# Kernel optimization log

Hardware: AMD Instinct MI355X
Metric: run time of the kernel (lower is better)

Reference implementation:

```python
import jax, jax.numpy as jnp
import numpy as np

B, S, T, V, E, H, D, A = 16, 128, 128, 32000, 512, 512, 512, 512
ENC = 2 * H  # bidirectional encoder output dim
NEG = -1e9


def _w(key, shape, scale=0.05):
    return scale * jax.random.normal(key, shape, dtype=jnp.float32)


def setup_inputs() -> dict:
    key = jax.random.key(0)
    ks = jax.random.split(key, 26)
    src = jax.random.randint(ks[0], (B, S), 1, V)
    tgt = jax.random.randint(ks[1], (B, T), 1, V)
    src_lens = jnp.full((B,), S, dtype=jnp.int32)  # full-length sequences (pack == identity)
    return dict(
        src=src, src_lens=src_lens, tgt=tgt,
        enc_embed=_w(ks[2], (V, E)).at[0].set(0.0),   # padding_idx=0
        Wih_f=_w(ks[3], (4 * H, E)), Whh_f=_w(ks[4], (4 * H, H)),
        bih_f=_w(ks[5], (4 * H,)), bhh_f=_w(ks[6], (4 * H,)),
        Wih_b=_w(ks[7], (4 * H, E)), Whh_b=_w(ks[8], (4 * H, H)),
        bih_b=_w(ks[9], (4 * H,)), bhh_b=_w(ks[10], (4 * H,)),
        Wbh=_w(ks[11], (D, 2 * H)), bbh=_w(ks[12], (D,)),
        Wbc=_w(ks[13], (D, 2 * H)), bbc=_w(ks[14], (D,)),
        Wh_att=_w(ks[15], (A, ENC)), Ws_att=_w(ks[16], (A, D)), v_att=_w(ks[17], (A,)),
        dec_embed=_w(ks[18], (V, E)).at[0].set(0.0),  # padding_idx=0
        Wih_d=_w(ks[19], (4 * D, E + ENC)), Whh_d=_w(ks[20], (4 * D, D)),
        bih_d=_w(ks[21], (4 * D,)), bhh_d=_w(ks[22], (4 * D,)),
        Wfc=_w(ks[23], (V, D + ENC)), bfc=_w(ks[24], (V,)),
    )


def _lstm_cell(x, h, c, Wih, Whh, bih, bhh):
    # PyTorch gate order: i, f, g, o
    g = x @ Wih.T + h @ Whh.T + (bih + bhh)
    i, f, gg, o = jnp.split(g, 4, axis=-1)
    c = jax.nn.sigmoid(f) * c + jax.nn.sigmoid(i) * jnp.tanh(gg)
    h = jax.nn.sigmoid(o) * jnp.tanh(c)
    return h, c


def _run_lstm(xs, Wih, Whh, bih, bhh, hdim):
    # xs: [S, B, E] -> (hs [S, B, hdim], h_last, c_last)
    b = xs.shape[1]
    h0 = jnp.zeros((b, hdim), xs.dtype)

    def step(carry, x):
        h, c = carry
        h, c = _lstm_cell(x, h, c, Wih, Whh, bih, bhh)
        return (h, c), h

    (hT, cT), hs = jax.lax.scan(step, (h0, h0), xs)
    return hs, hT, cT


def reference(src, src_lens, tgt, enc_embed, Wih_f, Whh_f, bih_f, bhh_f,
              Wih_b, Whh_b, bih_b, bhh_b, Wbh, bbh, Wbc, bbc,
              Wh_att, Ws_att, v_att, dec_embed, Wih_d, Whh_d, bih_d, bhh_d,
              Wfc, bfc):
    # ---- BiLSTM encoder (src_lens == S, so packing is the identity) ----
    emb = enc_embed[src]                      # [B, S, E]
    xs = jnp.swapaxes(emb, 0, 1)              # [S, B, E]
    hs_f, hf, _ = _run_lstm(xs, Wih_f, Whh_f, bih_f, bhh_f, H)
    hs_b, hb, _ = _run_lstm(xs[::-1], Wih_b, Whh_b, bih_b, bhh_b, H)
    hs_b = hs_b[::-1]
    enc_out = jnp.swapaxes(jnp.concatenate([hs_f, hs_b], axis=-1), 0, 1)  # [B, S, 2H]

    # ---- bridge (num_layers = 1) ----
    h_cat = jnp.concatenate([hf, hb], axis=-1)  # [B, 2H]
    h0 = jnp.tanh(h_cat @ Wbh.T + bbh)          # [B, D]
    c_cat = jnp.concatenate([hf, hb], axis=-1)
    c0 = jnp.tanh(c_cat @ Wbc.T + bbc)

    mask = jnp.arange(S)[None, :] < src_lens[:, None]  # [B, S]
    enc_proj = jnp.einsum('bse,ae->bsa', enc_out, Wh_att)  # W_h(enc_out), hoisted

    # ---- decoder loop, teacher_forcing = 1.0 ----
    def dec_step(carry, inp_t):
        h, c = carry
        # Bahdanau attention on top-layer hidden state
        score = jnp.einsum('bsa,a->bs', jnp.tanh(enc_proj + (h @ Ws_att.T)[:, None, :]), v_att)
        score = jnp.where(mask, score, NEG)
        attn = jax.nn.softmax(score, axis=-1)
        ctx = jnp.einsum('bs,bse->be', attn, enc_out)       # [B, 2H]
        x = jnp.concatenate([dec_embed[inp_t], ctx], axis=-1)  # [B, E+2H]
        h, c = _lstm_cell(x, h, c, Wih_d, Whh_d, bih_d, bhh_d)
        logits = jnp.concatenate([h, ctx], axis=-1) @ Wfc.T + bfc  # [B, V]
        return (h, c), logits

    inps = tgt[:, :-1].T  # [T-1, B]
    _, logits = jax.lax.scan(dec_step, (h0, c0), inps)
    return jnp.swapaxes(logits, 0, 1)  # [B, T-1, V]
```

## Files before the change

### kernel.cpp

```cpp
#include <hip/hip_runtime.h>

typedef __bf16 bf16x8 __attribute__((ext_vector_type(8)));
typedef float f32x4 __attribute__((ext_vector_type(4)));
typedef unsigned short us;
typedef unsigned long long ull;

#define DEV static __device__ __forceinline__

DEV float bf2f(us u){ union { unsigned u; float f; } x; x.u = ((unsigned)u) << 16; return x.f; }
DEV us f2bf(float f){
  union { float f; unsigned u; } x; x.f = f;
  unsigned r = x.u + 0x7fffu + ((x.u >> 16) & 1u);
  return (us)(r >> 16);
}
DEV unsigned pack2(us lo, us hi){ return (unsigned)lo | ((unsigned)hi << 16); }
DEV float sigm(float x){ return 1.0f / (1.0f + expf(-x)); }
DEV float tanh_fast(float x){ float e = __expf(2.0f * x); return 1.0f - 2.0f / (e + 1.0f); }
DEV void unpk2(unsigned u, float& a, float& b){ a = bf2f((us)u); b = bf2f((us)(u >> 16)); }

DEV unsigned ld4v(const unsigned* p){ return __hip_atomic_load(p, __ATOMIC_RELAXED, __HIP_MEMORY_SCOPE_AGENT); }
DEV ull ld8v(const void* p){ return __hip_atomic_load((const ull*)p, __ATOMIC_RELAXED, __HIP_MEMORY_SCOPE_AGENT); }
DEV void st4v(unsigned* p, unsigned v){ __hip_atomic_store(p, v, __ATOMIC_RELAXED, __HIP_MEMORY_SCOPE_AGENT); }

DEV void gridbar3(unsigned* arr, unsigned ep){
  __syncthreads();
  if (threadIdx.x == 0)
    __hip_atomic_store(arr + (size_t)blockIdx.x * 16, ep, __ATOMIC_RELEASE, __HIP_MEMORY_SCOPE_AGENT);
  if (threadIdx.x < 128){
    while (__hip_atomic_load(arr + (size_t)threadIdx.x * 16, __ATOMIC_RELAXED, __HIP_MEMORY_SCOPE_AGENT) < ep)
      __builtin_amdgcn_s_sleep(4);
  }
  __syncthreads();
}

DEV void groupbar(unsigned* gbase, int slot, unsigned ep){
  __syncthreads();
  if (threadIdx.x == 0)
    __hip_atomic_store(gbase + slot * 16, ep, __ATOMIC_RELEASE, __HIP_MEMORY_SCOPE_AGENT);
  if (threadIdx.x < 8){
    while (__hip_atomic_load(gbase + threadIdx.x * 16, __ATOMIC_RELAXED, __HIP_MEMORY_SCOPE_AGENT) < ep)
      __builtin_amdgcn_s_sleep(2);
  }
  __syncthreads();
}

__global__ void k_f2bf(const float4* __restrict__ in, uint2* __restrict__ out, long n4){
  long stride = (long)gridDim.x * blockDim.x;
  for (long i = (long)blockIdx.x * blockDim.x + threadIdx.x; i < n4; i += stride){
    float4 v = in[i];
    uint2 o; o.x = pack2(f2bf(v.x), f2bf(v.y)); o.y = pack2(f2bf(v.z), f2bf(v.w));
    out[i] = o;
  }
}

__global__ void k_bias3(const float* a0, const float* b0, float* o0,
                        const float* a1, const float* b1, float* o1,
                        const float* a2, const float* b2, float* o2){
  int i = blockIdx.x * 256 + threadIdx.x;
  o0[i] = a0[i] + b0[i];
  o1[i] = a1[i] + b1[i];
  o2[i] = a2[i] + b2[i];
}

__global__ void k_embed(const int* __restrict__ tok, const float* __restrict__ table,
                        us* __restrict__ out){
  int r = blockIdx.x;
  int b = r & 15, pos = r >> 4;
  int idx = tok[b * 128 + pos];
  float4 v = ((const float4*)(table + (size_t)idx * 512))[threadIdx.x];
  uint2 o; o.x = pack2(f2bf(v.x), f2bf(v.y)); o.y = pack2(f2bf(v.z), f2bf(v.w));
  ((uint2*)(out + (size_t)r * 512))[threadIdx.x] = o;
}

template<int MODE>
__global__ __launch_bounds__(256)
void gemm_bt(const us* __restrict__ A, int lda,
             const us* __restrict__ B, int ldb,
             const float* __restrict__ bias,
             void* __restrict__ Cv, int ldc, int K, int mvalid)
{
  __shared__ __align__(16) us As[128 * 64];
  __shared__ __align__(16) us Bs[128 * 64];
  const int tid  = threadIdx.x;
  const int lane = tid & 63, wid = tid >> 6;
  const int wm = (wid >> 1) * 64, wn = (wid & 1) * 64;
  const us* Ab = A + (size_t)blockIdx.y * 128 * lda;
  const us* Bb = B + (size_t)blockIdx.x * 128 * ldb;

  f32x4 acc[4][4] = {};
  bf16x8 ga[4], gb[4];

  #pragma unroll
  for (int r = 0; r < 4; r++){
    int c = tid + r * 256;
    ga[r] = *(const bf16x8*)(Ab + (size_t)(c >> 3) * lda + (c & 7) * 8);
    gb[r] = *(const bf16x8*)(Bb + (size_t)(c >> 3) * ldb + (c & 7) * 8);
  }
  const int nt = K >> 6;
  for (int t = 0; t < nt; t++){
    #pragma unroll
    for (int r = 0; r < 4; r++){
      int c = tid + r * 256;
      int slot = ((c >> 3) * 8 + ((c & 7) ^ ((c >> 3) & 7))) * 8;
      *(bf16x8*)(As + slot) = ga[r];
      *(bf16x8*)(Bs + slot) = gb[r];
    }
    __syncthreads();
    if (t + 1 < nt){
      int k0 = (t + 1) * 64;
      #pragma unroll
      for (int r = 0; r < 4; r++){
        int c = tid + r * 256;
        ga[r] = *(const bf16x8*)(Ab + (size_t)(c >> 3) * lda + k0 + (c & 7) * 8);
        gb[r] = *(const bf16x8*)(Bb + (size_t)(c >> 3) * ldb + k0 + (c & 7) * 8);
      }
    }
    #pragma unroll
    for (int kk = 0; kk < 2; kk++){
      bf16x8 av[4], bv[4];
      #pragma unroll
      for (int i = 0; i < 4; i++){
        int ra = wm + i * 16 + (lane & 15);
        int ua = (kk * 4 + (lane >> 4)) ^ (ra & 7);
        av[i] = *(const bf16x8*)(As + (ra * 8 + ua) * 8);
        int rb = wn + i * 16 + (lane & 15);
        int ub = (kk * 4 + (lane >> 4)) ^ (rb & 7);
        bv[i] = *(const bf16x8*)(Bs + (rb * 8 + ub) * 8);
      }
      #pragma unroll
      for (int i = 0; i < 4; i++)
        #pragma unroll
        for (int j = 0; j < 4; j++)
          acc[i][j] = __builtin_amdgcn_mfma_f32_16x16x32_bf16(av[i], bv[j], acc[i][j], 0, 0, 0);
    }
    if (t + 1 < nt) __syncthreads();
  }

  const int cb = lane & 15, rb4 = (lane >> 4) * 4;
  #pragma unroll
  for (int i = 0; i < 4; i++){
    #pragma unroll
    for (int j = 0; j < 4; j++){
      #pragma unroll
      for (int r = 0; r < 4; r++){
        int row = blockIdx.y * 128 + wm + i * 16 + rb4 + r;
        int col = blockIdx.x * 128 + wn + j * 16 + cb;
        float v = acc[i][j][r];
        if (bias) v += bias[col];
        if (MODE == 0) ((float*)Cv)[(size_t)row * ldc + col] = v;
        else           ((us*)Cv)[(size_t)row * ldc + col] = f2bf(v);
      }
    }
  }
}

__global__ __launch_bounds__(256)
void enc_persist4(const float* __restrict__ gin_f, const float* __restrict__ gin_b,
                  const us* __restrict__ whhf_bf, const us* __restrict__ whhb_bf,
                  us* __restrict__ enc_out_bf,
                  unsigned* __restrict__ arr)
{
  __shared__ __align__(16) us Wt[2][1024][8];
  __shared__ __align__(16) us Hrow[2][16][520];
  __shared__ __align__(16) f32x4 P[2][4][64];
  __shared__ float gl[2][16][17];
  __shared__ float hvout[2][16][4];

  const int bx = blockIdx.x, tid = threadIdx.x;
  const int lane = tid & 63, wv = tid >> 6;

  for (int d = 0; d < 2; d++){
    const us* srcw = d ? whhb_bf : whhf_bf;
    for (int u = tid; u < 1024; u += 256){
      int ks = u >> 6, ch = (u >> 4) & 3, v = u & 15;
      int n = (v & 3) * 512 + bx * 4 + (v >> 2);
      *(bf16x8*)Wt[d][u] = *(const bf16x8*)(srcw + (size_t)n * 512 + ks * 32 + ch * 8);
    }
  }

  float creg = 0.0f;
  const int cd = (tid >> 6) & 1, cb = tid & 15, cj = (tid >> 4) & 3;

  for (int t = 0; t < 128; t++){
    if (t == 0){
      #pragma unroll
      for (int r = 0; r < 8; r++){
        int u = tid + r * 256;
        int d = u >> 10, b = (u >> 6) & 15, s16 = u & 63;
        *(ull*)&Hrow[d][b][s16 * 8]     = 0ull;
        *(ull*)&Hrow[d][b][s16 * 8 + 4] = 0ull;
      }
    } else {
      #pragma unroll
      for (int r = 0; r < 8; r++){
        int u = tid + r * 256;
        int d = u >> 10, b = (u >> 6) & 15, s16 = u & 63;
        int sp = d ? (128 - t) : (t - 1);
        const us* s = enc_out_bf + ((size_t)b * 128 + sp) * 1024 + d * 512 + s16 * 8;
        ull lo = ld8v(s), hi = ld8v(s + 4);
        *(ull*)&Hrow[d][b][s16 * 8]     = lo;
        *(ull*)&Hrow[d][b][s16 * 8 + 4] = hi;
      }
    }
    __syncthreads();
    #pragma unroll
    for (int d = 0; d < 2; d++){
      f32x4 acc = {};
      #pragma unroll
      for (int m = 0; m < 4; m++){
        int ks = wv * 4 + m;
        int ch = lane >> 4, b = lane & 15;
        acc = __builtin_amdgcn_mfma_f32_16x16x32_bf16(*(const bf16x8*)&Hrow[d][b][ks * 32 + ch * 8],
                                                      *(const bf16x8*)Wt[d][(ks * 4 + ch) * 16 + b],
                                                      acc, 0, 0, 0);
      }
      P[d][wv][lane] = acc;
    }
    __syncthreads();
    if (wv < 2){
      int d = wv;
      f32x4 sum = (P[d][0][lane] + P[d][1][lane]) + (P[d][2][lane] + P[d][3][lane]);
      int v = lane & 15;
      int n = (v & 3) * 512 + bx * 4 + (v >> 2);
      int s_in = d ? (127 - t) : t;
      const float* gg = (d ? gin_b : gin_f) + (size_t)s_in * 16 * 2048 + n;
      #pragma unroll
      for (int r = 0; r < 4; r++){
        int b = (lane >> 4) * 4 + r;
        gl[d][v][b] = sum[r] + gg[(size_t)b * 2048];
      }
    }
    __syncthreads();
    if (tid < 128){
      float ig = sigm (gl[cd][cj * 4 + 0][cb]);
      float fg = sigm (gl[cd][cj * 4 + 1][cb]);
      float g2 = tanhf(gl[cd][cj * 4 + 2][cb]);
      float og = sigm (gl[cd][cj * 4 + 3][cb]);
      float cn = fg * creg + ig * g2;
      float hv = og * tanhf(cn);
      creg = cn;
      hvout[cd][cb][cj] = hv;
    }
    __syncthreads();
    if (tid < 64){
      int d = tid >> 5, rem = tid & 31, b = rem & 15, jp = rem >> 4;
      int s_in = d ? (127 - t) : t;
      st4v((unsigned*)(enc_out_bf + ((size_t)b * 128 + s_in) * 1024 + d * 512 + bx * 4 + jp * 2),
           pack2(f2bf(hvout[d][b][jp * 2]), f2bf(hvout[d][b][jp * 2 + 1])));
    }
    if (t != 127) gridbar3(arr, t + 1);
  }
}

__global__ __launch_bounds__(512)
void k_h0c0(const us* __restrict__ enc_out_bf, const float* __restrict__ Wbh, const float* __restrict__ bbh,
            const float* __restrict__ Wbc, const float* __restrict__ bbc,
            us* __restrict__ h0_bf, float* __restrict__ c_dec)
{
  __shared__ float hc[1024];
  int b = blockIdx.x >> 1, which = blockIdx.x & 1;
  int tid = threadIdx.x;
  hc[tid]       = bf2f(enc_out_bf[((size_t)b * 128 + 127) * 1024 + tid]);
  hc[512 + tid] = bf2f(enc_out_bf[((size_t)b * 128 + 0)   * 1024 + 512 + tid]);
  __syncthreads();
  const float* W = which ? Wbc : Wbh;
  float acc = (which ? bbc : bbh)[tid];
  const float* wr = W + (size_t)tid * 1024;
  for (int k = 0; k < 1024; k += 4){
    float4 w = *(const float4*)(wr + k);
    acc += w.x * hc[k] + w.y * hc[k + 1] + w.z * hc[k + 2] + w.w * hc[k + 3];
  }
  float v = tanhf(acc);
  if (which) c_dec[b * 512 + tid] = v;
  else       h0_bf[b * 512 + tid] = f2bf(v);
}

#define SMEM_BYTES 162464

__global__ __launch_bounds__(256)
void dec_fused3(const us* __restrict__ h0_bf, const float* __restrict__ c_dec0,
                const float* __restrict__ Ws_att, const float* __restrict__ v_att,
                const us* __restrict__ enc_proj_bf, const us* __restrict__ enc_out_bf,
                const int* __restrict__ src_lens, const float* __restrict__ gin_d,
                const us* __restrict__ whhd_bf, const us* __restrict__ wihd_bf,
                float* __restrict__ pscore_g,
                us* __restrict__ hctx,
                const us* __restrict__ wfc, const float* __restrict__ bfc,
                float* __restrict__ out,
                unsigned* __restrict__ arr, unsigned* __restrict__ arrG,
                unsigned* __restrict__ tdone)
{
  __shared__ __align__(16) char smem[SMEM_BYTES];
  const int tid = threadIdx.x;

  if (blockIdx.x >= 128){
    us* As = (us*)smem;
    us* Bs = (us*)(smem + 32768);
    const int lane = tid & 63, wid = tid >> 6;
    const int wm = wid * 64;
    for (int tile = blockIdx.x - 128; tile < 2000; tile += 128){
      int rt = tile / 250, ct = tile - rt * 250;
      unsigned need = (rt == 7) ? 127u : (unsigned)(16 * rt + 16);
      if (tid == 0){
        while (ld4v(tdone) < need) __builtin_amdgcn_s_sleep(8);
      }
      __syncthreads();
      const us* Ab = hctx + (size_t)rt * 256 * 1536;
      const us* Bb = wfc  + (size_t)ct * 128 * 1536;
      f32x4 acc[4][8] = {};
      bf16x8 ga[8], gb[4];
      #pragma unroll
      for (int r = 0; r < 8; r++){
        int cc = tid + r * 256;
        int row = cc >> 3, piece = cc & 7;
        bool val = (rt * 256 + row) < 2032;
        union { ull q[2]; bf16x8 v; } u;
        const us* p = Ab + (size_t)row * 1536 + piece * 8;
        u.q[0] = val ? ld8v(p) : 0ull;
        u.q[1] = val ? ld8v(p + 4) : 0ull;
        ga[r] = u.v;
      }
      #pragma unroll
      for (int r = 0; r < 4; r++){
        int cc = tid + r * 256;
        gb[r] = __builtin_nontemporal_load((const bf16x8*)(Bb + (size_t)(cc >> 3) * 1536 + (cc & 7) * 8));
      }
      for (int tk = 0; tk < 24; tk++){
        #pragma unroll
        for (int r = 0; r < 8; r++){
          int cc = tid + r * 256;
          int slot = ((cc >> 3) * 8 + ((cc & 7) ^ ((cc >> 3) & 7))) * 8;
          *(bf16x8*)(As + slot) = ga[r];
        }
        #pragma unroll
        for (int r = 0; r < 4; r++){
          int cc = tid + r * 256;
          int slot = ((cc >> 3) * 8 + ((cc & 7) ^ ((cc >> 3) & 7))) * 8;
          *(bf16x8*)(Bs + slot) = gb[r];
        }
        __syncthreads();
        if (tk + 1 < 24){
          int k0 = (tk + 1) * 64;
          #pragma unroll
          for (int r = 0; r < 8; r++){
            int cc = tid + r * 256;
            int row = cc >> 3, piece = cc & 7;
            bool val = (rt * 256 + row) < 2032;
            union { ull q[2]; bf16x8 v; } u;
            const us* p = Ab + (size_t)row * 1536 + k0 + piece * 8;
            u.q[0] = val ? ld8v(p) : 0ull;
            u.q[1] = val ? ld8v(p + 4) : 0ull;
            ga[r] = u.v;
          }
          #pragma unroll
          for (int r = 0; r < 4; r++){
            int cc = tid + r * 256;
            gb[r] = __builtin_nontemporal_load((const bf16x8*)(Bb + (size_t)(cc >> 3) * 1536 + k0 + (cc & 7) * 8));
          }
        }
        #pragma unroll
        for (int kk = 0; kk < 2; kk++){
          bf16x8 av[4], bv[8];
          #pragma unroll
          for (int i = 0; i < 4; i++){
            int ra = wm + i * 16 + (lane & 15);
            int ua = (kk * 4 + (lane >> 4)) ^ (ra & 7);
            av[i] = *(const bf16x8*)(As + (ra * 8 + ua) * 8);
          }
          #pragma unroll
          for (int j = 0; j < 8; j++){
            int rb = j * 16 + (lane & 15);
            int ub = (kk * 4 + (lane >> 4)) ^ (rb & 7);
            bv[j] = *(const bf16x8*)(Bs + (rb * 8 + ub) * 8);
          }
          #pragma unroll
          for (int i = 0; i < 4; i++)
            #pragma unroll
            for (int j = 0; j < 8; j++)
              acc[i][j] = __builtin_amdgcn_mfma_f32_16x16x32_bf16(av[i], bv[j], acc[i][j], 0, 0, 0);
        }
        if (tk + 1 < 24) __syncthreads();
      }
      const int cbl = lane & 15, rb4 = (lane >> 4) * 4;
      #pragma unroll
      for (int i = 0; i < 4; i++){
        #pragma unroll
        for (int j = 0; j < 8; j++){
          #pragma unroll
          for (int r = 0; r < 4; r++){
            int row = rt * 256 + wm + i * 16 + rb4 + r;
            int col = ct * 128 + j * 16 + cbl;
            if (row < 2032){
              float v = acc[i][j][r] + bfc[col];
              int tt = row >> 4, b = row & 15;
              out[((size_t)b * 127 + tt) * 32000 + col] = v;
            }
          }
        }
      }
    }
    return;
  }

  us (*Wh)[8]      = (us(*)[8])(smem);
  us (*Wc)[8]      = (us(*)[8])(smem + 16384);
  us (*Ws64)[520]  = (us(*)[520])(smem + 49152);
  us (*Xrow)[1032] = (us(*)[1032])(smem + 115712);
  f32x4 (*P)[64]   = (f32x4(*)[64])(smem + 148736);
  float (*g1l)[17] = (float(*)[17])(smem + 152832);
  float (*gl)[17]  = (float(*)[17])(smem + 153920);
  float* vl64      = (float*)(smem + 155008);
  float (*hsp)[64] = (float(*)[64])(smem + 155264);
  float* hs_own    = (float*)(smem + 156288);
  float (*pall)[128] = (float(*)[128])(smem + 156544);
  float* att       = (float*)(smem + 160640);
  float (*cred)[128] = (float(*)[128])(smem + 161152);
  float* sred      = (float*)(smem + 162176);
  float (*hvs)[4]  = (float(*)[4])(smem + 162208);

  const int bx = blockIdx.x;
  const int lane = tid & 63, wv = tid >> 6;
  const int bB = bx & 15, sQ = bx >> 4;
  unsigned* gbase = arrG + bB * 128;

  for (int u = tid; u < 1024; u += 256){
    int ks = u >> 6, ch = (u >> 4) & 3, v = u & 15;
    int n = (v & 3) * 512 + bx * 4 + (v >> 2);
    *(bf16x8*)Wh[u] = *(const bf16x8*)(whhd_bf + (size_t)n * 512 + ks * 32 + ch * 8);
  }
  for (int u = tid; u < 2048; u += 256){
    int ks = u >> 6, ch = (u >> 4) & 3, v = u & 15;
    int n = (v & 3) * 512 + bx * 4 + (v >> 2);
    *(bf16x8*)Wc[u] = *(const bf16x8*)(wihd_bf + (size_t)n * 1536 + 512 + ks * 32 + ch * 8);
  }
  for (int u = tid; u < 32768; u += 256){
    int a = u >> 9, k = u & 511;
    Ws64[a][k] = f2bf(Ws_att[(size_t)(sQ * 64 + a) * 512 + k]);
  }
  if (tid < 64) vl64[tid] = v_att[sQ * 64 + tid];
  const int slen = src_lens[bB];

  float creg = 0.0f;
  if (tid < 64) creg = c_dec0[(tid & 15) * 512 + bx * 4 + (tid >> 4)];

  for (int t = 0; t < 127; t++){
    const us* hsrc = t ? (hctx + (size_t)(t - 1) * 16 * 1536) : h0_bf;
    const int hstride = t ? 1536 : 512;

    #pragma unroll
    for (int r = 0; r < 4; r++){
      int u = tid + r * 256;
      int b = u >> 6, s16 = u & 63;
      const us* s = hsrc + (size_t)b * hstride + s16 * 8;
      ull lo = ld8v(s), hi = ld8v(s + 4);
      *(ull*)&Xrow[b][s16 * 8]     = lo;
      *(ull*)&Xrow[b][s16 * 8 + 4] = hi;
    }
    __syncthreads();
    {
      f32x4 acc = {};
      #pragma unroll
      for (int m = 0; m < 4; m++){
        int ks = wv * 4 + m;
        int ch = lane >> 4, b = lane & 15;
        acc = __builtin_amdgcn_mfma_f32_16x16x32_bf16(*(const bf16x8*)&Xrow[b][ks * 32 + ch * 8],
                                                      *(const bf16x8*)Wh[(ks * 4 + ch) * 16 + b],
                                                      acc, 0, 0, 0);
      }
      P[wv][lane] = acc;
    }
    {
      const us* wr = Ws64[lane] + wv * 128;
      const us* xr = Xrow[bB] + wv * 128;
      float s = 0.f;
      #pragma unroll
      for (int k = 0; k < 128; k += 8){
        bf16x8 xv = *(const bf16x8*)(xr + k);
        bf16x8 wv8 = *(const bf16x8*)(wr + k);
        #pragma unroll
        for (int e = 0; e < 8; e++) s += (float)xv[e] * (float)wv8[e];
      }
      hsp[wv][lane] = s;
    }
    __syncthreads();
    if (wv == 0){
      f32x4 sum = (P[0][lane] + P[1][lane]) + (P[2][lane] + P[3][lane]);
      int v = lane & 15;
      int n = (v & 3) * 512 + bx * 4 + (v >> 2);
      #pragma unroll
      for (int r = 0; r < 4; r++){
        int b = (lane >> 4) * 4 + r;
        g1l[v][b] = sum[r] + gin_d[((size_t)t * 16 + b) * 2048 + n];
      }
    }
    if (tid < 64) hs_own[tid] = hsp[0][tid] + hsp[1][tid] + hsp[2][tid] + hsp[3][tid];
    __syncthreads();
    {
      int s = tid >> 1, half = tid & 1;
      const us* er = enc_proj_bf + ((size_t)bB * 128 + s) * 512 + sQ * 64 + half * 32;
      const float* hb = hs_own + half * 32;
      const float* vp = vl64 + half * 32;
      float sv = 0.f;
      #pragma unroll
      for (int a = 0; a < 32; a += 8){
        uint4 u4 = *(const uint4*)(er + a);
        float e0,e1,e2,e3,e4,e5,e6,e7;
        unpk2(u4.x,e0,e1); unpk2(u4.y,e2,e3); unpk2(u4.z,e4,e5); unpk2(u4.w,e6,e7);
        sv += vp[a+0]*tanh_fast(e0+hb[a+0]) + vp[a+1]*tanh_fast(e1+hb[a+1])
            + vp[a+2]*tanh_fast(e2+hb[a+2]) + vp[a+3]*tanh_fast(e3+hb[a+3])
            + vp[a+4]*tanh_fast(e4+hb[a+4]) + vp[a+5]*tanh_fast(e5+hb[a+5])
            + vp[a+6]*tanh_fast(e6+hb[a+6]) + vp[a+7]*tanh_fast(e7+hb[a+7]);
      }
      sv += __shfl_xor(sv, 1);
      if (half == 0)
        st4v((unsigned*)&pscore_g[(size_t)bB * 1024 + sQ * 128 + s], __float_as_uint(sv));
    }

    groupbar(gbase, sQ, t + 1);

    for (int u = tid; u < 1024; u += 256)
      (&pall[0][0])[u] = __uint_as_float(ld4v((unsigned*)&pscore_g[(size_t)bB * 1024 + u]));
    __syncthreads();
    {
      float e = 0.f;
      if (tid < 128){
        float sc = ((pall[0][tid] + pall[1][tid]) + (pall[2][tid] + pall[3][tid]))
                 + ((pall[4][tid] + pall[5][tid]) + (pall[6][tid] + pall[7][tid]));
        e = (tid < slen) ? __expf(sc) : 0.f;
        att[tid] = e;
      }
      float ss = e;
      #pragma unroll
      for (int o = 32; o; o >>= 1) ss += __shfl_xor(ss, o);
      if (lane == 0) sred[wv] = ss;
    }
    __syncthreads();
    {
      int kk = tid & 127, half = tid >> 7;
      const float* ab = att + half * 64;
      const us* er = enc_out_bf + ((size_t)(bB * 128 + half * 64)) * 1024 + sQ * 128 + kk;
      float s = 0.f;
      #pragma unroll 8
      for (int s2 = 0; s2 < 64; s2++)
        s += ab[s2] * bf2f(er[(size_t)s2 * 1024]);
      cred[half][kk] = s;
    }
    __syncthreads();
    if (tid < 64){
      float inv = 1.0f / (sred[0] + sred[1] + sred[2] + sred[3]);
      int kk2 = tid * 2;
      float c0 = (cred[0][kk2]     + cred[1][kk2])     * inv;
      float c1 = (cred[0][kk2 + 1] + cred[1][kk2 + 1]) * inv;
      st4v((unsigned*)(hctx + ((size_t)t * 16 + bB) * 1536 + 512 + sQ * 128 + kk2),
           pack2(f2bf(c0), f2bf(c1)));
    }

    gridbar3(arr, 2 * t + 1);

    #pragma unroll
    for (int r = 0; r < 8; r++){
      int u = tid + r * 256;
      int b = u >> 7, s16 = u & 127;
      const us* s = hctx + ((size_t)t * 16 + b) * 1536 + 512 + s16 * 8;
      ull lo = ld8v(s), hi = ld8v(s + 4);
      *(ull*)&Xrow[b][s16 * 8]     = lo;
      *(ull*)&Xrow[b][s16 * 8 + 4] = hi;
    }
    __syncthreads();
    {
      f32x4 acc = {};
      #pragma unroll
      for (int m = 0; m < 8; m++){
        int ks = wv * 8 + m;
        int ch = lane >> 4, b = lane & 15;
        acc = __builtin_amdgcn_mfma_f32_16x16x32_bf16(*(const bf16x8*)&Xrow[b][ks * 32 + ch * 8],
                                                      *(const bf16x8*)Wc[(ks * 4 + ch) * 16 + b],
                                                      acc, 0, 0, 0);
      }
      P[wv][lane] = acc;
    }
    __syncthreads();
    if (wv == 0){
      f32x4 sum = (P[0][lane] + P[1][lane]) + (P[2][lane] + P[3][lane]);
      int v = lane & 15;
      #pragma unroll
      for (int r = 0; r < 4; r++){
        int b = (lane >> 4) * 4 + r;
        gl[v][b] = sum[r] + g1l[v][b];
      }
    }
    __syncthreads();
    if (tid < 64){
      int b2 = tid & 15, joff = tid >> 4;
      float ig = sigm (gl[joff * 4 + 0][b2]);
      float fg = sigm (gl[joff * 4 + 1][b2]);
      float g2 = tanhf(gl[joff * 4 + 2][b2]);
      float og = sigm (gl[joff * 4 + 3][b2]);
      float cn = fg * creg + ig * g2;
      float hv = og * tanhf(cn);
      creg = cn;
      hvs[b2][joff] = hv;
    }
    __syncthreads();
    if (tid < 32){
      int b = tid & 15, jp = tid >> 4;
      st4v((unsigned*)(hctx + ((size_t)t * 16 + b) * 1536 + bx * 4 + jp * 2),
           pack2(f2bf(hvs[b][jp * 2]), f2bf(hvs[b][jp * 2 + 1])));
    }
    gridbar3(arr, 2 * t + 2);
    if (bx == 0 && tid == 0)
      __hip_atomic_store(tdone, (unsigned)(t + 1), __ATOMIC_RELEASE, __HIP_MEMORY_SCOPE_AGENT);
  }
}

extern "C" void kernel_launch(void* const* d_in, const int* in_sizes, int n_in,
                              void* d_out, int out_size, void* d_ws, size_t ws_size,
                              hipStream_t stream)
{
  const int*   src       = (const int*)d_in[0];
  const int*   src_lens  = (const int*)d_in[1];
  const int*   tgt       = (const int*)d_in[2];
  const float* enc_embed = (const float*)d_in[3];
  const float* Wih_f = (const float*)d_in[4];
  const float* Whh_f = (const float*)d_in[5];
  const float* bih_f = (const float*)d_in[6];
  const float* bhh_f = (const float*)d_in[7];
  const float* Wih_b = (const float*)d_in[8];
  const float* Whh_b = (const float*)d_in[9];
  const float* bih_b = (const float*)d_in[10];
  const float* bhh_b = (const float*)d_in[11];
  const float* Wbh = (const float*)d_in[12];
  const float* bbh = (const float*)d_in[13];
  const float* Wbc = (const float*)d_in[14];
  const float* bbc = (const float*)d_in[15];
  const float* Wh_att = (const float*)d_in[16];
  const float* Ws_att = (const float*)d_in[17];
  const float* v_att  = (const float*)d_in[18];
  const float* dec_embed = (const float*)d_in[19];
  const float* Wih_d = (const float*)d_in[20];
  const float* Whh_d = (const float*)d_in[21];
  const float* bih_d = (const float*)d_in[22];
  const float* bhh_d = (const float*)d_in[23];
  const float* Wfc = (const float*)d_in[24];
  const float* bfc = (const float*)d_in[25];
  float* out = (float*)d_out;

  char* base = (char*)d_ws;
  size_t off = 0;
  auto take = [&](size_t bytes) -> char* {
    char* p = base + off;
    off += (bytes + 255) & ~(size_t)255;
    return p;
  };
  us* wfc_bf    = (us*)take((size_t)32000 * 1536 * 2);
  us* emb_e     = (us*)take((size_t)2048 * 512 * 2);
  us* emb_d     = (us*)take((size_t)2048 * 512 * 2);
  us* wihf_bf   = (us*)take((size_t)2048 * 512 * 2);
  us* wihb_bf   = (us*)take((size_t)2048 * 512 * 2);
  us* wihd_bf   = (us*)take((size_t)2048 * 1536 * 2);
  us* whhf_bf   = (us*)take((size_t)2048 * 512 * 2);
  us* whhb_bf   = (us*)take((size_t)2048 * 512 * 2);
  us* whhd_bf   = (us*)take((size_t)2048 * 512 * 2);
  us* whatt_bf  = (us*)take((size_t)512 * 1024 * 2);
  float* gin_f    = (float*)take((size_t)2048 * 2048 * 4);
  float* gin_b    = (float*)take((size_t)2048 * 2048 * 4);
  float* gin_d    = (float*)take((size_t)2048 * 2048 * 4);
  us* enc_out_bf  = (us*)take((size_t)2048 * 1024 * 2);
  us* enc_proj_bf = (us*)take((size_t)2048 * 512 * 2);
  us* hctx        = (us*)take((size_t)2048 * 1536 * 2);
  us* h0_bf       = (us*)take((size_t)16 * 512 * 2);
  float* c_dec    = (float*)take((size_t)16 * 512 * 4);
  float* pscore_g = (float*)take((size_t)16 * 1024 * 4);
  float* bias_f = (float*)take(2048 * 4);
  float* bias_b = (float*)take(2048 * 4);
  float* bias_d = (float*)take(2048 * 4);
  unsigned* arrE  = (unsigned*)take(128 * 16 * 4);
  unsigned* arrD  = (unsigned*)take(128 * 16 * 4);
  unsigned* arrG  = (unsigned*)take(16 * 8 * 16 * 4);
  unsigned* tdone = (unsigned*)take(256);

  hipMemsetAsync(emb_d, 0, (size_t)2048 * 512 * 2, stream);
  hipMemsetAsync(hctx, 0, (size_t)2048 * 1536 * 2, stream);
  hipMemsetAsync(arrE, 0, (128 * 16 + 128 * 16 + 16 * 8 * 16) * 4 + 256, stream);

  k_f2bf<<<4096, 256, 0, stream>>>((const float4*)Wfc,   (uint2*)wfc_bf,   (long)32000 * 1536 / 4);
  k_f2bf<<<512,  256, 0, stream>>>((const float4*)Wih_f, (uint2*)wihf_bf,  (long)2048 * 512 / 4);
  k_f2bf<<<512,  256, 0, stream>>>((const float4*)Wih_b, (uint2*)wihb_bf,  (long)2048 * 512 / 4);
  k_f2bf<<<1024, 256, 0, stream>>>((const float4*)Wih_d, (uint2*)wihd_bf,  (long)2048 * 1536 / 4);
  k_f2bf<<<512,  256, 0, stream>>>((const float4*)Whh_f, (uint2*)whhf_bf,  (long)2048 * 512 / 4);
  k_f2bf<<<512,  256, 0, stream>>>((const float4*)Whh_b, (uint2*)whhb_bf,  (long)2048 * 512 / 4);
  k_f2bf<<<512,  256, 0, stream>>>((const float4*)Whh_d, (uint2*)whhd_bf,  (long)2048 * 512 / 4);
  k_f2bf<<<512,  256, 0, stream>>>((const float4*)Wh_att,(uint2*)whatt_bf, (long)512 * 1024 / 4);
  k_bias3<<<8, 256, 0, stream>>>(bih_f, bhh_f, bias_f, bih_b, bhh_b, bias_b, bih_d, bhh_d, bias_d);

  k_embed<<<2048, 128, 0, stream>>>(src, enc_embed, emb_e);
  k_embed<<<2032, 128, 0, stream>>>(tgt, dec_embed, emb_d);

  gemm_bt<0><<<dim3(16, 16), 256, 0, stream>>>(emb_e, 512, wihf_bf, 512,  bias_f, gin_f, 2048, 512, 4096);
  gemm_bt<0><<<dim3(16, 16), 256, 0, stream>>>(emb_e, 512, wihb_bf, 512,  bias_b, gin_b, 2048, 512, 4096);
  gemm_bt<0><<<dim3(16, 16), 256, 0, stream>>>(emb_d, 512, wihd_bf, 1536, bias_d, gin_d, 2048, 512, 4096);

  enc_persist4<<<128, 256, 0, stream>>>(gin_f, gin_b, whhf_bf, whhb_bf, enc_out_bf, arrE);

  k_h0c0<<<32, 512, 0, stream>>>(enc_out_bf, Wbh, bbh, Wbc, bbc, h0_bf, c_dec);

  gemm_bt<2><<<dim3(4, 16), 256, 0, stream>>>(enc_out_bf, 1024, whatt_bf, 1024, nullptr, enc_proj_bf, 512, 1024, 4096);

  dec_fused3<<<256, 256, 0, stream>>>(h0_bf, c_dec, Ws_att, v_att, enc_proj_bf, enc_out_bf, src_lens,
                                      gin_d, whhd_bf, wihd_bf, pscore_g, hctx,
                                      wfc_bf, bfc, out, arrD, arrG, tdone);
}
```

Measured before the change: 3.678 ms.

## Precompute Wih_ctx·enc_out per batch so decoder gates use attention weights directly

Adds a GEMM that multiplies the context half of the decoder input weights by each batch's encoder outputs ahead of the decoder loop, giving a per-batch matrix M. Each step can then form the context gate term as attention weights times M, with no need to assemble the full context vector and run an MFMA over it. Attention exponentials are exchanged through a small global buffer, and the grid barriers are split into signal and wait halves so the recurrent MFMA overlaps the group barrier wait. The trade is an extra precompute kernel, a larger M buffer read from global memory every step, and normalisation moved after the projection.

```diff
diff --git a/kernel.cpp b/kernel.cpp
--- a/kernel.cpp
+++ b/kernel.cpp
@@ -22,27 +22,31 @@
 DEV ull ld8v(const void* p){ return __hip_atomic_load((const ull*)p, __ATOMIC_RELAXED, __HIP_MEMORY_SCOPE_AGENT); }
 DEV void st4v(unsigned* p, unsigned v){ __hip_atomic_store(p, v, __ATOMIC_RELAXED, __HIP_MEMORY_SCOPE_AGENT); }
 
-DEV void gridbar3(unsigned* arr, unsigned ep){
+DEV void barS(unsigned* arr, unsigned ep){
   __syncthreads();
   if (threadIdx.x == 0)
     __hip_atomic_store(arr + (size_t)blockIdx.x * 16, ep, __ATOMIC_RELEASE, __HIP_MEMORY_SCOPE_AGENT);
+}
+DEV void barW(unsigned* arr, unsigned ep){
   if (threadIdx.x < 128){
     while (__hip_atomic_load(arr + (size_t)threadIdx.x * 16, __ATOMIC_RELAXED, __HIP_MEMORY_SCOPE_AGENT) < ep)
       __builtin_amdgcn_s_sleep(4);
   }
   __syncthreads();
 }
-
-DEV void groupbar(unsigned* gbase, int slot, unsigned ep){
+DEV void gbarS(unsigned* gbase, int slot, unsigned ep){
   __syncthreads();
   if (threadIdx.x == 0)
     __hip_atomic_store(gbase + slot * 16, ep, __ATOMIC_RELEASE, __HIP_MEMORY_SCOPE_AGENT);
+}
+DEV void gbarW(unsigned* gbase, unsigned ep){
   if (threadIdx.x < 8){
     while (__hip_atomic_load(gbase + threadIdx.x * 16, __ATOMIC_RELAXED, __HIP_MEMORY_SCOPE_AGENT) < ep)
       __builtin_amdgcn_s_sleep(2);
   }
   __syncthreads();
 }
+DEV void gridbar3(unsigned* arr, unsigned ep){ barS(arr, ep); barW(arr, ep); }
 
 __global__ void k_f2bf(const float4* __restrict__ in, uint2* __restrict__ out, long n4){
   long stride = (long)gridDim.x * blockDim.x;
@@ -152,6 +156,76 @@
       }
     }
   }
+}
+
+__global__ __launch_bounds__(256)
+void gemm_M(const us* __restrict__ A, const us* __restrict__ B0, us* __restrict__ M)
+{
+  __shared__ __align__(16) us As[128 * 64];
+  __shared__ __align__(16) us Bs[128 * 64];
+  const int tid  = threadIdx.x;
+  const int lane = tid & 63, wid = tid >> 6;
+  const int wm = (wid >> 1) * 64, wn = (wid & 1) * 64;
+  const us* Ab = A + (size_t)blockIdx.y * 128 * 1536;
+  const us* Bb = B0 + (size_t)blockIdx.z * 131072;
+
+  f32x4 acc[4][4] = {};
+  bf16x8 ga[4], gb[4];
+  #pragma unroll
+  for (int r = 0; r < 4; r++){
+    int c = tid + r * 256;
+    ga[r] = *(const bf16x8*)(Ab + (size_t)(c >> 3) * 1536 + (c & 7) * 8);
+    gb[r] = *(const bf16x8*)(Bb + (size_t)(c >> 3) * 1024 + (c & 7) * 8);
+  }
+  for (int t = 0; t < 16; t++){
+    #pragma unroll
+    for (int r = 0; r < 4; r++){
+      int c = tid + r * 256;
+      int slot = ((c >> 3) * 8 + ((c & 7) ^ ((c >> 3) & 7))) * 8;
+      *(bf16x8*)(As + slot) = ga[r];
+      *(bf16x8*)(Bs + slot) = gb[r];
+    }
+    __syncthreads();
+    if (t + 1 < 16){
+      int k0 = (t + 1) * 64;
+      #pragma unroll
+      for (int r = 0; r < 4; r++){
+        int c = tid + r * 256;
+        ga[r] = *(const bf16x8*)(Ab + (size_t)(c >> 3) * 1536 + k0 + (c & 7) * 8);
+        gb[r] = *(const bf16x8*)(Bb + (size_t)(c >> 3) * 1024 + k0 + (c & 7) * 8);
+      }
+    }
+    #pragma unroll
+    for (int kk = 0; kk < 2; kk++){
+      bf16x8 av[4], bv[4];
+      #pragma unroll
+      for (int i = 0; i < 4; i++){
+        int ra = wm + i * 16 + (lane & 15);
+        int ua = (kk * 4 + (lane >> 4)) ^ (ra & 7);
+        av[i] = *(const bf16x8*)(As + (ra * 8 + ua) * 8);
+        int rb = wn + i * 16 + (lane & 15);
+        int ub = (kk * 4 + (lane >> 4)) ^ (rb & 7);
+        bv[i] = *(const bf16x8*)(Bs + (rb * 8 + ub) * 8);
+      }
+      #pragma unroll
+      for (int i = 0; i < 4; i++)
+        #pragma unroll
+        for (int j = 0; j < 4; j++)
+          acc[i][j] = __builtin_amdgcn_mfma_f32_16x16x32_bf16(av[i], bv[j], acc[i][j], 0, 0, 0);
+    }
+    if (t + 1 < 16) __syncthreads();
+  }
+  const int cb = lane & 15, rb4 = (lane >> 4) * 4;
+  #pragma unroll
+  for (int i = 0; i < 4; i++)
+    #pragma unroll
+    for (int j = 0; j < 4; j++)
+      #pragma unroll
+      for (int r = 0; r < 4; r++){
+        int row = blockIdx.y * 128 + wm + i * 16 + rb4 + r;
+        int col = wn + j * 16 + cb;
+        M[(size_t)row * 2048 + blockIdx.z * 128 + col] = f2bf(acc[i][j][r]);
+      }
 }
 
 __global__ __launch_bounds__(256)
@@ -275,15 +349,15 @@
   else       h0_bf[b * 512 + tid] = f2bf(v);
 }
 
-#define SMEM_BYTES 162464
+#define SMEM_BYTES 121856
 
 __global__ __launch_bounds__(256)
-void dec_fused3(const us* __restrict__ h0_bf, const float* __restrict__ c_dec0,
+void dec_fused4(const us* __restrict__ h0_bf, const float* __restrict__ c_dec0,
                 const float* __restrict__ Ws_att, const float* __restrict__ v_att,
                 const us* __restrict__ enc_proj_bf, const us* __restrict__ enc_out_bf,
                 const int* __restrict__ src_lens, const float* __restrict__ gin_d,
-                const us* __restrict__ whhd_bf, const us* __restrict__ wihd_bf,
-                float* __restrict__ pscore_g,
+                const us* __restrict__ whhd_bf, const us* __restrict__ Mmat,
+                float* __restrict__ pscore_g, float* __restrict__ att_g,
                 us* __restrict__ hctx,
                 const us* __restrict__ wfc, const float* __restrict__ bfc,
                 float* __restrict__ out,
@@ -403,20 +477,21 @@
   }
 
   us (*Wh)[8]      = (us(*)[8])(smem);
-  us (*Wc)[8]      = (us(*)[8])(smem + 16384);
-  us (*Ws64)[520]  = (us(*)[520])(smem + 49152);
-  us (*Xrow)[1032] = (us(*)[1032])(smem + 115712);
-  f32x4 (*P)[64]   = (f32x4(*)[64])(smem + 148736);
-  float (*g1l)[17] = (float(*)[17])(smem + 152832);
-  float (*gl)[17]  = (float(*)[17])(smem + 153920);
-  float* vl64      = (float*)(smem + 155008);
-  float (*hsp)[64] = (float(*)[64])(smem + 155264);
-  float* hs_own    = (float*)(smem + 156288);
-  float (*pall)[128] = (float(*)[128])(smem + 156544);
-  float* att       = (float*)(smem + 160640);
-  float (*cred)[128] = (float(*)[128])(smem + 161152);
-  float* sred      = (float*)(smem + 162176);
-  float (*hvs)[4]  = (float(*)[4])(smem + 162208);
+  us (*Ws64)[520]  = (us(*)[520])(smem + 16384);
+  us (*Xrow)[520]  = (us(*)[520])(smem + 82944);
+  f32x4 (*P)[64]   = (f32x4(*)[64])(smem + 99584);
+  float (*g1l)[17] = (float(*)[17])(smem + 103680);
+  float (*gl)[17]  = (float(*)[17])(smem + 104768);
+  float* vl64      = (float*)(smem + 105856);
+  float (*hsp)[64] = (float(*)[64])(smem + 106112);
+  float* hs_own    = (float*)(smem + 107136);
+  float (*pall)[128] = (float(*)[128])(smem + 107392);
+  float* e_own     = (float*)(smem + 111488);
+  float (*e_sm)[132] = (float(*)[132])(smem + 112000);
+  float* inv_sm    = (float*)(smem + 120448);
+  float (*cred)[128] = (float(*)[128])(smem + 120512);
+  float* sred      = (float*)(smem + 121536);
+  float (*hvs)[4]  = (float(*)[4])(smem + 121568);
 
   const int bx = blockIdx.x;
   const int lane = tid & 63, wv = tid >> 6;
@@ -428,17 +503,16 @@
     int n = (v & 3) * 512 + bx * 4 + (v >> 2);
     *(bf16x8*)Wh[u] = *(const bf16x8*)(whhd_bf + (size_t)n * 512 + ks * 32 + ch * 8);
   }
-  for (int u = tid; u < 2048; u += 256){
-    int ks = u >> 6, ch = (u >> 4) & 3, v = u & 15;
-    int n = (v & 3) * 512 + bx * 4 + (v >> 2);
-    *(bf16x8*)Wc[u] = *(const bf16x8*)(wihd_bf + (size_t)n * 1536 + 512 + ks * 32 + ch * 8);
-  }
   for (int u = tid; u < 32768; u += 256){
     int a = u >> 9, k = u & 511;
     Ws64[a][k] = f2bf(Ws_att[(size_t)(sQ * 64 + a) * 512 + k]);
   }
   if (tid < 64) vl64[tid] = v_att[sQ * 64 + tid];
   const int slen = src_lens[bB];
+
+  const int vIdx = tid >> 4, bIdx = tid & 15;
+  const int nOwn = (vIdx & 3) * 512 + bx * 4 + (vIdx >> 2);
+  const us* Mrow = Mmat + (size_t)nOwn * 2048 + bIdx * 128;
 
   float creg = 0.0f;
   if (tid < 64) creg = c_dec0[(tid & 15) * 512 + bx * 4 + (tid >> 4)];
@@ -458,18 +532,6 @@
     }
     __syncthreads();
     {
-      f32x4 acc = {};
-      #pragma unroll
-      for (int m = 0; m < 4; m++){
-        int ks = wv * 4 + m;
-        int ch = lane >> 4, b = lane & 15;
-        acc = __builtin_amdgcn_mfma_f32_16x16x32_bf16(*(const bf16x8*)&Xrow[b][ks * 32 + ch * 8],
-                                                      *(const bf16x8*)Wh[(ks * 4 + ch) * 16 + b],
-                                                      acc, 0, 0, 0);
-      }
-      P[wv][lane] = acc;
-    }
-    {
       const us* wr = Ws64[lane] + wv * 128;
       const us* xr = Xrow[bB] + wv * 128;
       float s = 0.f;
@@ -483,16 +545,6 @@
       hsp[wv][lane] = s;
     }
     __syncthreads();
-    if (wv == 0){
-      f32x4 sum = (P[0][lane] + P[1][lane]) + (P[2][lane] + P[3][lane]);
-      int v = lane & 15;
-      int n = (v & 3) * 512 + bx * 4 + (v >> 2);
-      #pragma unroll
-      for (int r = 0; r < 4; r++){
-        int b = (lane >> 4) * 4 + r;
-        g1l[v][b] = sum[r] + gin_d[((size_t)t * 16 + b) * 2048 + n];
-      }
-    }
     if (tid < 64) hs_own[tid] = hsp[0][tid] + hsp[1][tid] + hsp[2][tid] + hsp[3][tid];
     __syncthreads();
     {
@@ -515,8 +567,32 @@
       if (half == 0)
         st4v((unsigned*)&pscore_g[(size_t)bB * 1024 + sQ * 128 + s], __float_as_uint(sv));
     }
-
-    groupbar(gbase, sQ, t + 1);
+    gbarS(gbase, sQ, t + 1);
+
+    {
+      f32x4 acc = {};
+      #pragma unroll
+      for (int m = 0; m < 4; m++){
+        int ks = wv * 4 + m;
+        int ch = lane >> 4, b = lane & 15;
+        acc = __builtin_amdgcn_mfma_f32_16x16x32_bf16(*(const bf16x8*)&Xrow[b][ks * 32 + ch * 8],
+                                                      *(const bf16x8*)Wh[(ks * 4 + ch) * 16 + b],
+                                                      acc, 0, 0, 0);
+      }
+      P[wv][lane] = acc;
+    }
+    __syncthreads();
+    if (wv == 0){
+      f32x4 sum = (P[0][lane] + P[1][lane]) + (P[2][lane] + P[3][lane]);
+      int v = lane & 15;
+      int n = (v & 3) * 512 + bx * 4 + (v >> 2);
+      #pragma unroll
+      for (int r = 0; r < 4; r++){
+        int b = (lane >> 4) * 4 + r;
+        g1l[v][b] = sum[r] + gin_d[((size_t)t * 16 + b) * 2048 + n];
+      }
+    }
+    gbarW(gbase, t + 1);
 
     for (int u = tid; u < 1024; u += 256)
       (&pall[0][0])[u] = __uint_as_float(ld4v((unsigned*)&pscore_g[(size_t)bB * 1024 + u]));
@@ -527,17 +603,20 @@
         float sc = ((pall[0][tid] + pall[1][tid]) + (pall[2][tid] + pall[3][tid]))
                  + ((pall[4][tid] + pall[5][tid]) + (pall[6][tid] + pall[7][tid]));
         e = (tid < slen) ? __expf(sc) : 0.f;
-        att[tid] = e;
+        e_own[tid] = e;
+        if ((tid >> 4) == sQ)
+          st4v((unsigned*)&att_g[bB * 128 + tid], __float_as_uint(e));
       }
       float ss = e;
       #pragma unroll
       for (int o = 32; o; o >>= 1) ss += __shfl_xor(ss, o);
-      if (lane == 0) sred[wv] = ss;
-    }
-    __syncthreads();
+      if (lane == 0 && wv < 2) sred[wv] = ss;
+    }
+    barS(arr, 2 * t + 1);
+
     {
       int kk = tid & 127, half = tid >> 7;
-      const float* ab = att + half * 64;
+      const float* ab = e_own + half * 64;
       const us* er = enc_out_bf + ((size_t)(bB * 128 + half * 64)) * 1024 + sQ * 128 + kk;
       float s = 0.f;
       #pragma unroll 8
@@ -547,47 +626,49 @@
     }
     __syncthreads();
     if (tid < 64){
-      float inv = 1.0f / (sred[0] + sred[1] + sred[2] + sred[3]);
+      float inv = 1.0f / (sred[0] + sred[1]);
       int kk2 = tid * 2;
       float c0 = (cred[0][kk2]     + cred[1][kk2])     * inv;
       float c1 = (cred[0][kk2 + 1] + cred[1][kk2 + 1]) * inv;
       st4v((unsigned*)(hctx + ((size_t)t * 16 + bB) * 1536 + 512 + sQ * 128 + kk2),
            pack2(f2bf(c0), f2bf(c1)));
     }
-
-    gridbar3(arr, 2 * t + 1);
-
-    #pragma unroll
-    for (int r = 0; r < 8; r++){
-      int u = tid + r * 256;
-      int b = u >> 7, s16 = u & 127;
-      const us* s = hctx + ((size_t)t * 16 + b) * 1536 + 512 + s16 * 8;
-      ull lo = ld8v(s), hi = ld8v(s + 4);
-      *(ull*)&Xrow[b][s16 * 8]     = lo;
-      *(ull*)&Xrow[b][s16 * 8 + 4] = hi;
+    barW(arr, 2 * t + 1);
+
+    for (int u = tid; u < 2048; u += 256){
+      int b = u >> 7, s = u & 127;
+      e_sm[b][s] = __uint_as_float(ld4v((unsigned*)&att_g[b * 128 + s]));
     }
     __syncthreads();
     {
-      f32x4 acc = {};
-      #pragma unroll
-      for (int m = 0; m < 8; m++){
-        int ks = wv * 8 + m;
-        int ch = lane >> 4, b = lane & 15;
-        acc = __builtin_amdgcn_mfma_f32_16x16x32_bf16(*(const bf16x8*)&Xrow[b][ks * 32 + ch * 8],
-                                                      *(const bf16x8*)Wc[(ks * 4 + ch) * 16 + b],
-                                                      acc, 0, 0, 0);
-      }
-      P[wv][lane] = acc;
-    }
-    __syncthreads();
-    if (wv == 0){
-      f32x4 sum = (P[0][lane] + P[1][lane]) + (P[2][lane] + P[3][lane]);
-      int v = lane & 15;
-      #pragma unroll
-      for (int r = 0; r < 4; r++){
-        int b = (lane >> 4) * 4 + r;
-        gl[v][b] = sum[r] + g1l[v][b];
-      }
+      float* dred = &cred[0][0];
+      if (tid < 128){
+        int b = tid >> 3, oct = tid & 7;
+        float s = 0.f;
+        #pragma unroll
+        for (int i = 0; i < 16; i++) s += e_sm[b][oct * 16 + i];
+        dred[b * 8 + oct] = s;
+      }
+      __syncthreads();
+      if (tid < 16){
+        float s = 0.f;
+        #pragma unroll
+        for (int i = 0; i < 8; i++) s += dred[tid * 8 + i];
+        inv_sm[tid] = 1.0f / s;
+      }
+    }
+    __syncthreads();
+    {
+      float acc = 0.f;
+      const float* eb = e_sm[bIdx];
+      #pragma unroll
+      for (int s8 = 0; s8 < 16; s8++){
+        bf16x8 m = *(const bf16x8*)(Mrow + s8 * 8);
+        #pragma unroll
+        for (int e = 0; e < 8; e++)
+          acc += eb[s8 * 8 + e] * (float)m[e];
+      }
+      gl[vIdx][bIdx] = acc * inv_sm[bIdx] + g1l[vIdx][bIdx];
     }
     __syncthreads();
     if (tid < 64){
@@ -607,7 +688,8 @@
       st4v((unsigned*)(hctx + ((size_t)t * 16 + b) * 1536 + bx * 4 + jp * 2),
            pack2(f2bf(hvs[b][jp * 2]), f2bf(hvs[b][jp * 2 + 1])));
     }
-    gridbar3(arr, 2 * t + 2);
+    barS(arr, 2 * t + 2);
+    barW(arr, 2 * t + 2);
     if (bx == 0 && tid == 0)
       __hip_atomic_store(tdone, (unsigned)(t + 1), __ATOMIC_RELEASE, __HIP_MEMORY_SCOPE_AGENT);
   }
@@ -662,6 +744,7 @@
   us* whhb_bf   = (us*)take((size_t)2048 * 512 * 2);
   us* whhd_bf   = (us*)take((size_t)2048 * 512 * 2);
   us* whatt_bf  = (us*)take((size_t)512 * 1024 * 2);
+  us* Mmat      = (us*)take((size_t)2048 * 16 * 128 * 2);
   float* gin_f    = (float*)take((size_t)2048 * 2048 * 4);
   float* gin_b    = (float*)take((size_t)2048 * 2048 * 4);
   float* gin_d    = (float*)take((size_t)2048 * 2048 * 4);
@@ -671,6 +754,7 @@
   us* h0_bf       = (us*)take((size_t)16 * 512 * 2);
   float* c_dec    = (float*)take((size_t)16 * 512 * 4);
   float* pscore_g = (float*)take((size_t)16 * 1024 * 4);
+  float* att_g    = (float*)take((size_t)16 * 128 * 4);
   float* bias_f = (float*)take(2048 * 4);
   float* bias_b = (float*)take(2048 * 4);
   float* bias_d = (float*)take(2048 * 4);
@@ -706,7 +790,9 @@
 
   gemm_bt<2><<<dim3(4, 16), 256, 0, stream>>>(enc_out_bf, 1024, whatt_bf, 1024, nullptr, enc_proj_bf, 512, 1024, 4096);
 
-  dec_fused3<<<256, 256, 0, stream>>>(h0_bf, c_dec, Ws_att, v_att, enc_proj_bf, enc_out_bf, src_lens,
-                                      gin_d, whhd_bf, wihd_bf, pscore_g, hctx,
+  gemm_M<<<dim3(1, 16, 16), 256, 0, stream>>>(wihd_bf + 512, enc_out_bf, Mmat);
+
+  dec_fused4<<<256, 256, 0, stream>>>(h0_bf, c_dec, Ws_att, v_att, enc_proj_bf, enc_out_bf, src_lens,
+                                      gin_d, whhd_bf, Mmat, pscore_g, att_g, hctx,
                                       wfc_bf, bfc, out, arrD, arrG, tdone);
 }
```

New measurement: 3.998 ms. 8.7% more time.
